# Kernel optimization log

Measured on AMD Instinct MI355X. Metric: run time of the kernel, lower is better.

## Reference

```python
import jax, jax.numpy as jnp
import numpy as np

FFT_LEN = 512
HOP_LEN = 256
N_BLOCK = 4
N_BIN = FFT_LEN // 2 + 1  # 257
STATE_FACTOR = 0.99999
ALPHA_E = 0.7
BETA_F = 0.1
BATCH = 4096
N_MIC = 1


def setup_inputs() -> dict:
    key = jax.random.key(0)
    ks = jax.random.split(key, 7)
    return {
        "mic": jax.random.normal(ks[0], (BATCH, HOP_LEN, N_MIC), jnp.float32),
        "loudspeaker_buffer": jax.random.normal(ks[1], (BATCH, (N_BLOCK + 1) * HOP_LEN), jnp.float32),
        "phi_e": jax.random.uniform(ks[2], (BATCH, N_BIN, N_MIC), jnp.float32),
        "phi_f": jax.random.uniform(ks[3], (BATCH, N_BIN, N_BLOCK, N_MIC), jnp.float32),
        "P1": jax.random.uniform(ks[4], (BATCH, N_BIN, N_BLOCK, N_MIC), jnp.float32),
        "H_post_real": 0.1 * jax.random.normal(ks[5], (BATCH, N_BIN, N_BLOCK, N_MIC), jnp.float32),
        "H_post_imag": 0.1 * jax.random.normal(ks[6], (BATCH, N_BIN, N_BLOCK, N_MIC), jnp.float32),
    }


def reference(mic, loudspeaker_buffer, phi_e, phi_f, P1, H_post_real, H_post_imag):
    B = mic.shape[0]
    sf2 = STATE_FACTOR * STATE_FACTOR
    H_post = jax.lax.complex(H_post_real, H_post_imag)  # [B, n_bin, n_block, n_mic]

    # STFT of loudspeaker buffer: rectangular window, center=False -> n_block frames
    frame_idx = jnp.arange(N_BLOCK)[:, None] * HOP_LEN + jnp.arange(FFT_LEN)[None, :]
    frames = loudspeaker_buffer[:, frame_idx]              # [B, n_block, fft_len]
    X = jnp.swapaxes(jnp.fft.rfft(frames, axis=-1), 1, 2)  # [B, n_bin, n_block]

    # zero-padded rFFT of mic frame
    zpad = jnp.zeros((B, FFT_LEN - HOP_LEN, N_MIC), mic.dtype)
    fd_mic = jnp.fft.rfft(jnp.concatenate([zpad, mic], axis=1), n=FFT_LEN, axis=1)  # [B, n_bin, n_mic]

    H_prior = H_post
    # a-priori feedback estimate
    fd_fb_hat = jnp.sum(X[..., None] * H_prior, axis=2)                     # [B, n_bin, n_mic]
    est_fb = jnp.fft.irfft(fd_fb_hat, FFT_LEN, axis=1)[:, HOP_LEN:, :]      # [B, hop, n_mic]
    fd_est_fb = jnp.fft.rfft(jnp.concatenate([zpad, est_fb], axis=1), n=FFT_LEN, axis=1)
    E = fd_mic - fd_est_fb                                                  # [B, n_bin, n_mic]

    phi_e = ALPHA_E * phi_e + (1.0 - ALPHA_E) * jnp.abs(E) ** 2

    # Kalman gain
    phi_f = BETA_F * phi_f + (1.0 - BETA_F) * jnp.abs(H_prior) ** 2
    phi_n = (1.0 - sf2) * phi_f
    Xr = jnp.abs(X) ** 2                                                    # [B, n_bin, n_block]
    U = Xr[..., None] * P1                                                  # [B, n_bin, n_block, n_mic]
    R = U + 2.0 * phi_e[:, :, None, :] + 1e-10
    K = P1 * jnp.conj(X)[..., None] / R                                     # [B, n_bin, n_block, n_mic]
    P0 = jax.lax.stop_gradient(P1) - 0.5 * jax.lax.stop_gradient(jnp.abs(K) ** 2 * R)
    P1_new = sf2 * P0 + phi_n  # state update (not part of returned output)

    # filter update via gradient-constrained overlap-save
    dH = jnp.fft.irfft(K * E[:, :, None, :], FFT_LEN, axis=1)               # [B, fft_len, n_block, n_mic]
    mask = (jnp.arange(FFT_LEN) < HOP_LEN).astype(dH.dtype)[None, :, None, None]
    fd_dH = jnp.fft.rfft(dH * mask, n=FFT_LEN, axis=1)                      # [B, n_bin, n_block, n_mic]
    H_post_new = STATE_FACTOR * (H_prior + fd_dH)

    # a-posteriori feedback estimate and enhanced frame
    fd_fb_hat2 = jnp.sum(X[..., None] * H_post_new, axis=2)
    est_fb2 = jnp.fft.irfft(fd_fb_hat2, FFT_LEN, axis=1)[:, HOP_LEN:, :]
    enhanced = mic - est_fb2                                                # [B, hop, n_mic]
    return enhanced
```

## Files before the change

kernel.cpp:

```cpp
#include <hip/hip_runtime.h>
#include <math.h>

#define SF 0.99999f
#define PI2 6.283185307179586476925f
#define SWZ(c) ((c) ^ (((c) >> 4) & 15))
#define LDSFENCE() asm volatile("" ::: "memory")

template<int SGN>
__device__ __forceinline__ void twmul(float& ur, float& ui, float c, float s) {
    const float ss = (SGN < 0) ? -s : s;
    const float r = ur * c - ui * ss;
    const float i = ui * c + ur * ss;
    ur = r; ui = i;
}

template<int SGN>
__device__ __forceinline__ void bfly8(float* ur, float* ui) {
    const float C2 = 0.70710678118654752440f;
    float ar[4], ai[4], br[4], bi[4];
#pragma unroll
    for (int m = 0; m < 4; ++m) {
        ar[m] = ur[m] + ur[m + 4]; ai[m] = ui[m] + ui[m + 4];
        br[m] = ur[m] - ur[m + 4]; bi[m] = ui[m] - ui[m + 4];
    }
    float b1r, b1i, b2r, b2i, b3r, b3i;
    if (SGN < 0) {
        b1r = C2 * (br[1] + bi[1]); b1i = C2 * (bi[1] - br[1]);
        b2r = bi[2];                b2i = -br[2];
        b3r = C2 * (bi[3] - br[3]); b3i = -C2 * (br[3] + bi[3]);
    } else {
        b1r = C2 * (br[1] - bi[1]); b1i = C2 * (bi[1] + br[1]);
        b2r = -bi[2];               b2i = br[2];
        b3r = -C2 * (br[3] + bi[3]); b3i = C2 * (br[3] - bi[3]);
    }
    const float e0r = ar[0] + ar[2], e0i = ai[0] + ai[2];
    const float e1r = ar[0] - ar[2], e1i = ai[0] - ai[2];
    const float o0r = ar[1] + ar[3], o0i = ai[1] + ai[3];
    const float o1r = ar[1] - ar[3], o1i = ai[1] - ai[3];
    ur[0] = e0r + o0r; ui[0] = e0i + o0i;
    ur[4] = e0r - o0r; ui[4] = e0i - o0i;
    if (SGN < 0) { ur[2] = e1r + o1i; ui[2] = e1i - o1r; ur[6] = e1r - o1i; ui[6] = e1i + o1r; }
    else         { ur[2] = e1r - o1i; ui[2] = e1i + o1r; ur[6] = e1r + o1i; ui[6] = e1i - o1r; }
    const float f0r = br[0] + b2r, f0i = bi[0] + b2i;
    const float f1r = br[0] - b2r, f1i = bi[0] - b2i;
    const float g0r = b1r + b3r, g0i = b1i + b3i;
    const float g1r = b1r - b3r, g1i = b1i - b3i;
    ur[1] = f0r + g0r; ui[1] = f0i + g0i;
    ur[5] = f0r - g0r; ui[5] = f0i - g0i;
    if (SGN < 0) { ur[3] = f1r + g1i; ui[3] = f1i - g1r; ur[7] = f1r - g1i; ui[7] = f1i + g1r; }
    else         { ur[3] = f1r - g1i; ui[3] = f1i + g1r; ur[7] = f1r + g1i; ui[7] = f1i - g1r; }
}

template<int SGN>
__device__ __forceinline__ void fft512w(float* ur, float* ui,
                                        float2* __restrict__ buf,
                                        const float2* __restrict__ tw2,
                                        const float2* __restrict__ tw3,
                                        int t) {
    bfly8<SGN>(ur, ui);
    LDSFENCE();
#pragma unroll
    for (int m = 0; m < 8; ++m) buf[SWZ(8 * t + m)] = make_float2(ur[m], ui[m]);
    LDSFENCE();
#pragma unroll
    for (int m = 0; m < 8; ++m) { const float2 v = buf[SWZ(t + 64 * m)]; ur[m] = v.x; ui[m] = v.y; }
    const int k2 = t & 7;
#pragma unroll
    for (int m = 1; m < 8; ++m) { const float2 w = tw2[m * 8 + k2]; twmul<SGN>(ur[m], ui[m], w.x, w.y); }
    bfly8<SGN>(ur, ui);
    const int jj = ((t >> 3) << 6) + k2;
    LDSFENCE();
#pragma unroll
    for (int m = 0; m < 8; ++m) buf[SWZ(jj + 8 * m)] = make_float2(ur[m], ui[m]);
    LDSFENCE();
#pragma unroll
    for (int m = 0; m < 8; ++m) { const float2 v = buf[SWZ(t + 64 * m)]; ur[m] = v.x; ui[m] = v.y; }
#pragma unroll
    for (int m = 1; m < 8; ++m) { const float2 w = tw3[m * 64 + t]; twmul<SGN>(ur[m], ui[m], w.x, w.y); }
    bfly8<SGN>(ur, ui);
    LDSFENCE();
}

__global__ __launch_bounds__(256, 2) void pbfd_kernel(
    const float* __restrict__ g_mic,
    const float* __restrict__ g_lsb,
    const float* __restrict__ g_phie,
    const float* __restrict__ g_p1,
    const float* __restrict__ g_hr,
    const float* __restrict__ g_hi,
    float* __restrict__ g_out,
    int B) {
    __shared__ float2 tw2[64];
    __shared__ float2 tw3[512];
    __shared__ float2 xch[4][512];
    __shared__ float nyq[4][14];

    const int tid = threadIdx.x;
    const int w = tid >> 6;
    const int t = tid & 63;
    const int elem = blockIdx.x * 4 + w;
    const int ec = (elem < B) ? elem : (B - 1);
    const int ml = (64 - t) & 63;

    float u[20];
    {
        const float* lb = g_lsb + (size_t)ec * 1280;
#pragma unroll
        for (int m = 0; m < 20; ++m) u[m] = lb[t + 64 * m];
    }
    float hr_[4][4], hi_[4][4];
    {
        const float4* hr4 = (const float4*)g_hr + (size_t)ec * 257;
        const float4* hi4 = (const float4*)g_hi + (size_t)ec * 257;
#pragma unroll
        for (int m = 0; m < 4; ++m) {
            const float4 a = hr4[t + 64 * m];
            hr_[0][m] = a.x; hr_[1][m] = a.y; hr_[2][m] = a.z; hr_[3][m] = a.w;
        }
#pragma unroll
        for (int m = 0; m < 4; ++m) {
            const float4 b = hi4[t + 64 * m];
            hi_[0][m] = b.x; hi_[1][m] = b.y; hi_[2][m] = b.z; hi_[3][m] = b.w;
        }
    }
    float mv[4];
    {
        const float* mp = g_mic + (size_t)ec * 256;
#pragma unroll
        for (int q = 0; q < 4; ++q) mv[q] = mp[t + 64 * q];
    }
    float phv[4];
    {
        const float* php = g_phie + (size_t)ec * 257;
#pragma unroll
        for (int m = 0; m < 4; ++m) phv[m] = php[t + 64 * m];
    }
    float4 p1q[4];
    {
        const float4* p14 = (const float4*)g_p1 + (size_t)ec * 257;
#pragma unroll
        for (int m = 0; m < 4; ++m) p1q[m] = p14[t + 64 * m];
    }
    float4 hnl = make_float4(0.f, 0.f, 0.f, 0.f), pnl = make_float4(0.f, 0.f, 0.f, 0.f);
    float ph256 = 0.f;
    if (t == 0) {
        hnl = ((const float4*)g_hr)[(size_t)ec * 257 + 256];
        pnl = ((const float4*)g_p1)[(size_t)ec * 257 + 256];
        ph256 = g_phie[(size_t)ec * 257 + 256];
    }

    for (int e = tid; e < 512; e += 256) {
        const int m = e >> 6, tt = e & 63;
        float s, c;
        sincosf(PI2 * (float)(m * tt) * (1.0f / 512.0f), &s, &c);
        tw3[e] = make_float2(c, s);
    }
    if (tid < 64) {
        const int m = tid >> 3, k = tid & 7;
        float s, c;
        sincosf(PI2 * (float)(m * k) * (1.0f / 64.0f), &s, &c);
        tw2[tid] = make_float2(c, s);
    }
    __syncthreads();

    float2* buf = &xch[w][0];
    float* ny = &nyq[w][0];
    if (t == 0) {
        ny[4] = hnl.x; ny[5] = hnl.y; ny[6] = hnl.z; ny[7] = hnl.w;
        ny[8] = pnl.x; ny[9] = pnl.y; ny[10] = pnl.z; ny[11] = pnl.w;
        ny[12] = ph256;
    }
    LDSFENCE();

    float xr[4][4], xi[4][4];
#pragma unroll
    for (int pr = 0; pr < 2; ++pr) {
        float ur[8], ui[8];
#pragma unroll
        for (int m = 0; m < 8; ++m) { ur[m] = u[8 * pr + m]; ui[m] = u[8 * pr + m + 4]; }
        fft512w<-1>(ur, ui, buf, tw2, tw3, t);
#pragma unroll
        for (int m = 0; m < 4; ++m) {
            float zmr = __shfl(ur[7 - m], ml);
            float zmi = __shfl(ui[7 - m], ml);
            if (t == 0) {
                zmr = (m == 0) ? ur[0] : ur[8 - m];
                zmi = (m == 0) ? ui[0] : ui[8 - m];
            }
            xr[2 * pr][m]     = 0.5f * (ur[m] + zmr);
            xi[2 * pr][m]     = 0.5f * (ui[m] - zmi);
            xr[2 * pr + 1][m] = 0.5f * (ui[m] + zmi);
            xi[2 * pr + 1][m] = -0.5f * (ur[m] - zmr);
        }
        if (t == 0) { ny[0 + 2 * pr] = ur[4]; ny[1 + 2 * pr] = ui[4]; }
        LDSFENCE();
    }

    auto sum_ifft = [&](float o4[4]) {
        float ur[8], ui[8];
#pragma unroll
        for (int m = 0; m < 4; ++m) {
            float cr = 0.f, ci = 0.f;
#pragma unroll
            for (int j = 0; j < 4; ++j) {
                cr += xr[j][m] * hr_[j][m] - xi[j][m] * hi_[j][m];
                ci += xr[j][m] * hi_[j][m] + xi[j][m] * hr_[j][m];
            }
            ur[m] = cr; ui[m] = ci;
        }
#pragma unroll
        for (int m = 4; m < 8; ++m) {
            const float cr = __shfl(ur[7 - m], ml);
            const float ci = __shfl(ui[7 - m], ml);
            ur[m] = cr; ui[m] = -ci;
        }
        if (t == 0) {
            ur[5] = ur[3]; ui[5] = -ui[3];
            ur[6] = ur[2]; ui[6] = -ui[2];
            ur[7] = ur[1]; ui[7] = -ui[1];
            float cn = 0.f;
#pragma unroll
            for (int j = 0; j < 4; ++j) cn += ny[j] * ny[4 + j];
            ur[4] = cn; ui[4] = 0.f;
        }
        fft512w<1>(ur, ui, buf, tw2, tw3, t);
#pragma unroll
        for (int q = 0; q < 4; ++q) o4[q] = ur[4 + q] * (1.0f / 512.0f);
    };

    float d4[4];
    {
        float o4[4];
        sum_ifft(o4);
#pragma unroll
        for (int q = 0; q < 4; ++q) d4[q] = mv[q] - o4[q];
    }

    float er[4], ei[4];
    {
        float ur[8], ui[8];
#pragma unroll
        for (int m = 0; m < 4; ++m) { ur[m] = 0.f; ui[m] = 0.f; }
#pragma unroll
        for (int q = 0; q < 4; ++q) { ur[4 + q] = d4[q]; ui[4 + q] = 0.f; }
        fft512w<-1>(ur, ui, buf, tw2, tw3, t);
#pragma unroll
        for (int m = 0; m < 4; ++m) { er[m] = ur[m]; ei[m] = ui[m]; }
        if (t == 0) {
            const float en = ur[4];
            ny[13] = en;
            ny[12] = 0.7f * ny[12] + 0.3f * en * en;
        }
        LDSFENCE();
    }

    float pe[4];
#pragma unroll
    for (int m = 0; m < 4; ++m)
        pe[m] = 0.7f * phv[m] + 0.3f * (er[m] * er[m] + ei[m] * ei[m]);

#pragma unroll
    for (int pr = 0; pr < 2; ++pr) {
        const int j0 = 2 * pr, j1 = 2 * pr + 1;
        float ur[8], ui[8], gr[4], gi[4];
#pragma unroll
        for (int m = 0; m < 4; ++m) {
            const float pa = pr ? p1q[m].z : p1q[m].x;
            const float pb = pr ? p1q[m].w : p1q[m].y;
            const float xxa = xr[j0][m] * xr[j0][m] + xi[j0][m] * xi[j0][m];
            const float Ra = xxa * pa + 2.f * pe[m] + 1e-10f;
            const float ia = 1.f / Ra;
            const float kra = pa * xr[j0][m] * ia, kia = -pa * xi[j0][m] * ia;
            const float a_r = kra * er[m] - kia * ei[m];
            const float a_i = kra * ei[m] + kia * er[m];
            const float xxb = xr[j1][m] * xr[j1][m] + xi[j1][m] * xi[j1][m];
            const float Rb = xxb * pb + 2.f * pe[m] + 1e-10f;
            const float ib = 1.f / Rb;
            const float krb = pb * xr[j1][m] * ib, kib = -pb * xi[j1][m] * ib;
            const float b_r = krb * er[m] - kib * ei[m];
            const float b_i = krb * ei[m] + kib * er[m];
            ur[m] = a_r - b_i;  ui[m] = a_i + b_r;
            gr[m] = a_r + b_i;  gi[m] = b_r - a_i;
        }
#pragma unroll
        for (int m = 4; m < 8; ++m) {
            ur[m] = __shfl(gr[7 - m], ml);
            ui[m] = __shfl(gi[7 - m], ml);
        }
        if (t == 0) {
            ur[5] = gr[3]; ui[5] = gi[3];
            ur[6] = gr[2]; ui[6] = gi[2];
            ur[7] = gr[1]; ui[7] = gi[1];
            const float xn0 = ny[j0], xn1 = ny[j1];
            const float pn0 = ny[8 + j0], pn1 = ny[8 + j1];
            const float en = ny[13], pen = ny[12];
            const float Rn0 = xn0 * xn0 * pn0 + 2.f * pen + 1e-10f;
            const float Rn1 = xn1 * xn1 * pn1 + 2.f * pen + 1e-10f;
            ur[4] = pn0 * xn0 / Rn0 * en;
            ui[4] = pn1 * xn1 / Rn1 * en;
        }
        fft512w<1>(ur, ui, buf, tw2, tw3, t);
#pragma unroll
        for (int m = 0; m < 4; ++m) { ur[m] *= (1.0f / 512.0f); ui[m] *= (1.0f / 512.0f); }
#pragma unroll
        for (int m = 4; m < 8; ++m) { ur[m] = 0.f; ui[m] = 0.f; }
        fft512w<-1>(ur, ui, buf, tw2, tw3, t);
#pragma unroll
        for (int m = 0; m < 4; ++m) {
            float zmr = __shfl(ur[7 - m], ml);
            float zmi = __shfl(ui[7 - m], ml);
            if (t == 0) {
                zmr = (m == 0) ? ur[0] : ur[8 - m];
                zmi = (m == 0) ? ui[0] : ui[8 - m];
            }
            const float f0r = 0.5f * (ur[m] + zmr), f0i = 0.5f * (ui[m] - zmi);
            const float f1r = 0.5f * (ui[m] + zmi), f1i = -0.5f * (ur[m] - zmr);
            hr_[j0][m] = SF * (hr_[j0][m] + f0r);
            hi_[j0][m] = SF * (hi_[j0][m] + f0i);
            hr_[j1][m] = SF * (hr_[j1][m] + f1r);
            hi_[j1][m] = SF * (hi_[j1][m] + f1i);
        }
        if (t == 0) {
            ny[4 + j0] = SF * (ny[4 + j0] + ur[4]);
            ny[4 + j1] = SF * (ny[4 + j1] + ui[4]);
        }
        LDSFENCE();
    }

    {
        float o4[4];
        sum_ifft(o4);
        if (elem < B) {
            float* op = g_out + (size_t)elem * 256;
#pragma unroll
            for (int q = 0; q < 4; ++q) op[t + 64 * q] = mv[q] - o4[q];
        }
    }
}

extern "C" void kernel_launch(void* const* d_in, const int* in_sizes, int n_in,
                              void* d_out, int out_size, void* d_ws, size_t ws_size,
                              hipStream_t stream) {
    const float* mic  = (const float*)d_in[0];
    const float* lsb  = (const float*)d_in[1];
    const float* phie = (const float*)d_in[2];
    const float* p1   = (const float*)d_in[4];
    const float* hr   = (const float*)d_in[5];
    const float* hi   = (const float*)d_in[6];
    float* out = (float*)d_out;

    const int B = in_sizes[0] / 256;
    const int blocks = (B + 3) / 4;
    pbfd_kernel<<<blocks, 256, 0, stream>>>(mic, lsb, phie, p1, hr, hi, out, B);
}
```

Baseline: 40.37 us.

## Interleave paired FFTs with dual LDS buffers and stagger wave start times

Adds a dual FFT routine that runs two independent 512-point FFTs at once using separate LDS scratch buffers. The loudspeaker STFT and the two filter-update FFT pairs now use it instead of running back to back, giving more instruction-level parallelism and overlapped LDS latency. It also raises the launch-bounds occupancy hint from 2 to 3 blocks per SM and inserts per-wave s_sleep offsets so waves do not all hit the same phase at once. The costs are doubled LDS scratch per wave, more live registers under a tighter register cap (risk of spills), and added sleep latency.

```diff
diff --git a/kernel.cpp b/kernel.cpp
--- a/kernel.cpp
+++ b/kernel.cpp
@@ -81,7 +81,58 @@
     LDSFENCE();
 }
 
-__global__ __launch_bounds__(256, 2) void pbfd_kernel(
+template<int SGN>
+__device__ __forceinline__ void fft512w_dual(float* urA, float* uiA,
+                                             float* urB, float* uiB,
+                                             float2* __restrict__ bufA,
+                                             float2* __restrict__ bufB,
+                                             const float2* __restrict__ tw2,
+                                             const float2* __restrict__ tw3,
+                                             int t) {
+    bfly8<SGN>(urA, uiA);
+    bfly8<SGN>(urB, uiB);
+    LDSFENCE();
+#pragma unroll
+    for (int m = 0; m < 8; ++m) bufA[SWZ(8 * t + m)] = make_float2(urA[m], uiA[m]);
+#pragma unroll
+    for (int m = 0; m < 8; ++m) bufB[SWZ(8 * t + m)] = make_float2(urB[m], uiB[m]);
+    LDSFENCE();
+#pragma unroll
+    for (int m = 0; m < 8; ++m) { const float2 v = bufA[SWZ(t + 64 * m)]; urA[m] = v.x; uiA[m] = v.y; }
+#pragma unroll
+    for (int m = 0; m < 8; ++m) { const float2 v = bufB[SWZ(t + 64 * m)]; urB[m] = v.x; uiB[m] = v.y; }
+    const int k2 = t & 7;
+#pragma unroll
+    for (int m = 1; m < 8; ++m) {
+        const float2 wv = tw2[m * 8 + k2];
+        twmul<SGN>(urA[m], uiA[m], wv.x, wv.y);
+        twmul<SGN>(urB[m], uiB[m], wv.x, wv.y);
+    }
+    bfly8<SGN>(urA, uiA);
+    bfly8<SGN>(urB, uiB);
+    const int jj = ((t >> 3) << 6) + k2;
+    LDSFENCE();
+#pragma unroll
+    for (int m = 0; m < 8; ++m) bufA[SWZ(jj + 8 * m)] = make_float2(urA[m], uiA[m]);
+#pragma unroll
+    for (int m = 0; m < 8; ++m) bufB[SWZ(jj + 8 * m)] = make_float2(urB[m], uiB[m]);
+    LDSFENCE();
+#pragma unroll
+    for (int m = 0; m < 8; ++m) { const float2 v = bufA[SWZ(t + 64 * m)]; urA[m] = v.x; uiA[m] = v.y; }
+#pragma unroll
+    for (int m = 0; m < 8; ++m) { const float2 v = bufB[SWZ(t + 64 * m)]; urB[m] = v.x; uiB[m] = v.y; }
+#pragma unroll
+    for (int m = 1; m < 8; ++m) {
+        const float2 wv = tw3[m * 64 + t];
+        twmul<SGN>(urA[m], uiA[m], wv.x, wv.y);
+        twmul<SGN>(urB[m], uiB[m], wv.x, wv.y);
+    }
+    bfly8<SGN>(urA, uiA);
+    bfly8<SGN>(urB, uiB);
+    LDSFENCE();
+}
+
+__global__ __launch_bounds__(256, 3) void pbfd_kernel(
     const float* __restrict__ g_mic,
     const float* __restrict__ g_lsb,
     const float* __restrict__ g_phie,
@@ -92,7 +143,7 @@
     int B) {
     __shared__ float2 tw2[64];
     __shared__ float2 tw3[512];
-    __shared__ float2 xch[4][512];
+    __shared__ float2 xch[4][2][512];
     __shared__ float nyq[4][14];
 
     const int tid = threadIdx.x;
@@ -108,6 +159,12 @@
 #pragma unroll
         for (int m = 0; m < 20; ++m) u[m] = lb[t + 64 * m];
     }
+    float mv[4];
+    {
+        const float* mp = g_mic + (size_t)ec * 256;
+#pragma unroll
+        for (int q = 0; q < 4; ++q) mv[q] = mp[t + 64 * q];
+    }
     float hr_[4][4], hi_[4][4];
     {
         const float4* hr4 = (const float4*)g_hr + (size_t)ec * 257;
@@ -122,12 +179,6 @@
             const float4 b = hi4[t + 64 * m];
             hi_[0][m] = b.x; hi_[1][m] = b.y; hi_[2][m] = b.z; hi_[3][m] = b.w;
         }
-    }
-    float mv[4];
-    {
-        const float* mp = g_mic + (size_t)ec * 256;
-#pragma unroll
-        for (int q = 0; q < 4; ++q) mv[q] = mp[t + 64 * q];
     }
     float phv[4];
     {
@@ -163,7 +214,8 @@
     }
     __syncthreads();
 
-    float2* buf = &xch[w][0];
+    float2* bufA = &xch[w][0][0];
+    float2* bufB = &xch[w][1][0];
     float* ny = &nyq[w][0];
     if (t == 0) {
         ny[4] = hnl.x; ny[5] = hnl.y; ny[6] = hnl.z; ny[7] = hnl.w;
@@ -172,27 +224,47 @@
     }
     LDSFENCE();
 
+    switch ((w + ((blockIdx.x & 1) << 2)) & 7) {
+        case 1: __builtin_amdgcn_s_sleep(2); break;
+        case 2: __builtin_amdgcn_s_sleep(4); break;
+        case 3: __builtin_amdgcn_s_sleep(6); break;
+        case 4: __builtin_amdgcn_s_sleep(8); break;
+        case 5: __builtin_amdgcn_s_sleep(10); break;
+        case 6: __builtin_amdgcn_s_sleep(12); break;
+        case 7: __builtin_amdgcn_s_sleep(14); break;
+        default: break;
+    }
+
     float xr[4][4], xi[4][4];
-#pragma unroll
-    for (int pr = 0; pr < 2; ++pr) {
-        float ur[8], ui[8];
-#pragma unroll
-        for (int m = 0; m < 8; ++m) { ur[m] = u[8 * pr + m]; ui[m] = u[8 * pr + m + 4]; }
-        fft512w<-1>(ur, ui, buf, tw2, tw3, t);
-#pragma unroll
-        for (int m = 0; m < 4; ++m) {
-            float zmr = __shfl(ur[7 - m], ml);
-            float zmi = __shfl(ui[7 - m], ml);
-            if (t == 0) {
-                zmr = (m == 0) ? ur[0] : ur[8 - m];
-                zmi = (m == 0) ? ui[0] : ui[8 - m];
-            }
-            xr[2 * pr][m]     = 0.5f * (ur[m] + zmr);
-            xi[2 * pr][m]     = 0.5f * (ui[m] - zmi);
-            xr[2 * pr + 1][m] = 0.5f * (ui[m] + zmi);
-            xi[2 * pr + 1][m] = -0.5f * (ur[m] - zmr);
-        }
-        if (t == 0) { ny[0 + 2 * pr] = ur[4]; ny[1 + 2 * pr] = ui[4]; }
+    {
+        float urA[8], uiA[8], urB[8], uiB[8];
+#pragma unroll
+        for (int m = 0; m < 8; ++m) {
+            urA[m] = u[m];     uiA[m] = u[m + 4];
+            urB[m] = u[m + 8]; uiB[m] = u[m + 12];
+        }
+        fft512w_dual<-1>(urA, uiA, urB, uiB, bufA, bufB, tw2, tw3, t);
+#pragma unroll
+        for (int m = 0; m < 4; ++m) {
+            float zmr = __shfl(urA[7 - m], ml);
+            float zmi = __shfl(uiA[7 - m], ml);
+            if (t == 0) { zmr = (m == 0) ? urA[0] : urA[8 - m]; zmi = (m == 0) ? uiA[0] : uiA[8 - m]; }
+            xr[0][m] = 0.5f * (urA[m] + zmr);
+            xi[0][m] = 0.5f * (uiA[m] - zmi);
+            xr[1][m] = 0.5f * (uiA[m] + zmi);
+            xi[1][m] = -0.5f * (urA[m] - zmr);
+        }
+#pragma unroll
+        for (int m = 0; m < 4; ++m) {
+            float zmr = __shfl(urB[7 - m], ml);
+            float zmi = __shfl(uiB[7 - m], ml);
+            if (t == 0) { zmr = (m == 0) ? urB[0] : urB[8 - m]; zmi = (m == 0) ? uiB[0] : uiB[8 - m]; }
+            xr[2][m] = 0.5f * (urB[m] + zmr);
+            xi[2][m] = 0.5f * (uiB[m] - zmi);
+            xr[3][m] = 0.5f * (uiB[m] + zmi);
+            xi[3][m] = -0.5f * (urB[m] - zmr);
+        }
+        if (t == 0) { ny[0] = urA[4]; ny[1] = uiA[4]; ny[2] = urB[4]; ny[3] = uiB[4]; }
         LDSFENCE();
     }
 
@@ -223,7 +295,7 @@
             for (int j = 0; j < 4; ++j) cn += ny[j] * ny[4 + j];
             ur[4] = cn; ui[4] = 0.f;
         }
-        fft512w<1>(ur, ui, buf, tw2, tw3, t);
+        fft512w<1>(ur, ui, bufA, tw2, tw3, t);
 #pragma unroll
         for (int q = 0; q < 4; ++q) o4[q] = ur[4 + q] * (1.0f / 512.0f);
     };
@@ -243,7 +315,7 @@
         for (int m = 0; m < 4; ++m) { ur[m] = 0.f; ui[m] = 0.f; }
 #pragma unroll
         for (int q = 0; q < 4; ++q) { ur[4 + q] = d4[q]; ui[4 + q] = 0.f; }
-        fft512w<-1>(ur, ui, buf, tw2, tw3, t);
+        fft512w<-1>(ur, ui, bufA, tw2, tw3, t);
 #pragma unroll
         for (int m = 0; m < 4; ++m) { er[m] = ur[m]; ei[m] = ui[m]; }
         if (t == 0) {
@@ -259,70 +331,104 @@
     for (int m = 0; m < 4; ++m)
         pe[m] = 0.7f * phv[m] + 0.3f * (er[m] * er[m] + ei[m] * ei[m]);
 
-#pragma unroll
-    for (int pr = 0; pr < 2; ++pr) {
-        const int j0 = 2 * pr, j1 = 2 * pr + 1;
-        float ur[8], ui[8], gr[4], gi[4];
-#pragma unroll
-        for (int m = 0; m < 4; ++m) {
-            const float pa = pr ? p1q[m].z : p1q[m].x;
-            const float pb = pr ? p1q[m].w : p1q[m].y;
-            const float xxa = xr[j0][m] * xr[j0][m] + xi[j0][m] * xi[j0][m];
-            const float Ra = xxa * pa + 2.f * pe[m] + 1e-10f;
-            const float ia = 1.f / Ra;
-            const float kra = pa * xr[j0][m] * ia, kia = -pa * xi[j0][m] * ia;
-            const float a_r = kra * er[m] - kia * ei[m];
-            const float a_i = kra * ei[m] + kia * er[m];
-            const float xxb = xr[j1][m] * xr[j1][m] + xi[j1][m] * xi[j1][m];
-            const float Rb = xxb * pb + 2.f * pe[m] + 1e-10f;
-            const float ib = 1.f / Rb;
-            const float krb = pb * xr[j1][m] * ib, kib = -pb * xi[j1][m] * ib;
-            const float b_r = krb * er[m] - kib * ei[m];
-            const float b_i = krb * ei[m] + kib * er[m];
-            ur[m] = a_r - b_i;  ui[m] = a_i + b_r;
-            gr[m] = a_r + b_i;  gi[m] = b_r - a_i;
+    {
+        float urA[8], uiA[8], urB[8], uiB[8];
+        float grA[4], giA[4], grB[4], giB[4];
+#pragma unroll
+        for (int m = 0; m < 4; ++m) {
+            const float xx0 = xr[0][m] * xr[0][m] + xi[0][m] * xi[0][m];
+            const float R0 = xx0 * p1q[m].x + 2.f * pe[m] + 1e-10f;
+            const float i0 = 1.f / R0;
+            const float kr0 = p1q[m].x * xr[0][m] * i0, ki0 = -p1q[m].x * xi[0][m] * i0;
+            const float a_r = kr0 * er[m] - ki0 * ei[m];
+            const float a_i = kr0 * ei[m] + ki0 * er[m];
+            const float xx1 = xr[1][m] * xr[1][m] + xi[1][m] * xi[1][m];
+            const float R1 = xx1 * p1q[m].y + 2.f * pe[m] + 1e-10f;
+            const float i1 = 1.f / R1;
+            const float kr1 = p1q[m].y * xr[1][m] * i1, ki1 = -p1q[m].y * xi[1][m] * i1;
+            const float b_r = kr1 * er[m] - ki1 * ei[m];
+            const float b_i = kr1 * ei[m] + ki1 * er[m];
+            urA[m] = a_r - b_i;  uiA[m] = a_i + b_r;
+            grA[m] = a_r + b_i;  giA[m] = b_r - a_i;
+
+            const float xx2 = xr[2][m] * xr[2][m] + xi[2][m] * xi[2][m];
+            const float R2 = xx2 * p1q[m].z + 2.f * pe[m] + 1e-10f;
+            const float i2 = 1.f / R2;
+            const float kr2 = p1q[m].z * xr[2][m] * i2, ki2 = -p1q[m].z * xi[2][m] * i2;
+            const float c_r = kr2 * er[m] - ki2 * ei[m];
+            const float c_i = kr2 * ei[m] + ki2 * er[m];
+            const float xx3 = xr[3][m] * xr[3][m] + xi[3][m] * xi[3][m];
+            const float R3 = xx3 * p1q[m].w + 2.f * pe[m] + 1e-10f;
+            const float i3 = 1.f / R3;
+            const float kr3 = p1q[m].w * xr[3][m] * i3, ki3 = -p1q[m].w * xi[3][m] * i3;
+            const float d_r = kr3 * er[m] - ki3 * ei[m];
+            const float d_i = kr3 * ei[m] + ki3 * er[m];
+            urB[m] = c_r - d_i;  uiB[m] = c_i + d_r;
+            grB[m] = c_r + d_i;  giB[m] = d_r - c_i;
         }
 #pragma unroll
         for (int m = 4; m < 8; ++m) {
-            ur[m] = __shfl(gr[7 - m], ml);
-            ui[m] = __shfl(gi[7 - m], ml);
+            urA[m] = __shfl(grA[7 - m], ml);
+            uiA[m] = __shfl(giA[7 - m], ml);
+            urB[m] = __shfl(grB[7 - m], ml);
+            uiB[m] = __shfl(giB[7 - m], ml);
         }
         if (t == 0) {
-            ur[5] = gr[3]; ui[5] = gi[3];
-            ur[6] = gr[2]; ui[6] = gi[2];
-            ur[7] = gr[1]; ui[7] = gi[1];
-            const float xn0 = ny[j0], xn1 = ny[j1];
-            const float pn0 = ny[8 + j0], pn1 = ny[8 + j1];
+            urA[5] = grA[3]; uiA[5] = giA[3];
+            urA[6] = grA[2]; uiA[6] = giA[2];
+            urA[7] = grA[1]; uiA[7] = giA[1];
+            urB[5] = grB[3]; uiB[5] = giB[3];
+            urB[6] = grB[2]; uiB[6] = giB[2];
+            urB[7] = grB[1]; uiB[7] = giB[1];
             const float en = ny[13], pen = ny[12];
-            const float Rn0 = xn0 * xn0 * pn0 + 2.f * pen + 1e-10f;
-            const float Rn1 = xn1 * xn1 * pn1 + 2.f * pen + 1e-10f;
-            ur[4] = pn0 * xn0 / Rn0 * en;
-            ui[4] = pn1 * xn1 / Rn1 * en;
-        }
-        fft512w<1>(ur, ui, buf, tw2, tw3, t);
-#pragma unroll
-        for (int m = 0; m < 4; ++m) { ur[m] *= (1.0f / 512.0f); ui[m] *= (1.0f / 512.0f); }
-#pragma unroll
-        for (int m = 4; m < 8; ++m) { ur[m] = 0.f; ui[m] = 0.f; }
-        fft512w<-1>(ur, ui, buf, tw2, tw3, t);
-#pragma unroll
-        for (int m = 0; m < 4; ++m) {
-            float zmr = __shfl(ur[7 - m], ml);
-            float zmi = __shfl(ui[7 - m], ml);
-            if (t == 0) {
-                zmr = (m == 0) ? ur[0] : ur[8 - m];
-                zmi = (m == 0) ? ui[0] : ui[8 - m];
+#pragma unroll
+            for (int j = 0; j < 4; ++j) {
+                const float xnj = ny[j], pnj = ny[8 + j];
+                const float Rn = xnj * xnj * pnj + 2.f * pen + 1e-10f;
+                const float ke = pnj * xnj / Rn * en;
+                if (j == 0) urA[4] = ke;
+                else if (j == 1) uiA[4] = ke;
+                else if (j == 2) urB[4] = ke;
+                else uiB[4] = ke;
             }
-            const float f0r = 0.5f * (ur[m] + zmr), f0i = 0.5f * (ui[m] - zmi);
-            const float f1r = 0.5f * (ui[m] + zmi), f1i = -0.5f * (ur[m] - zmr);
-            hr_[j0][m] = SF * (hr_[j0][m] + f0r);
-            hi_[j0][m] = SF * (hi_[j0][m] + f0i);
-            hr_[j1][m] = SF * (hr_[j1][m] + f1r);
-            hi_[j1][m] = SF * (hi_[j1][m] + f1i);
+        }
+        fft512w_dual<1>(urA, uiA, urB, uiB, bufA, bufB, tw2, tw3, t);
+#pragma unroll
+        for (int m = 0; m < 4; ++m) {
+            urA[m] *= (1.0f / 512.0f); uiA[m] *= (1.0f / 512.0f);
+            urB[m] *= (1.0f / 512.0f); uiB[m] *= (1.0f / 512.0f);
+        }
+#pragma unroll
+        for (int m = 4; m < 8; ++m) {
+            urA[m] = 0.f; uiA[m] = 0.f;
+            urB[m] = 0.f; uiB[m] = 0.f;
+        }
+        fft512w_dual<-1>(urA, uiA, urB, uiB, bufA, bufB, tw2, tw3, t);
+#pragma unroll
+        for (int m = 0; m < 4; ++m) {
+            float zmr = __shfl(urA[7 - m], ml);
+            float zmi = __shfl(uiA[7 - m], ml);
+            if (t == 0) { zmr = (m == 0) ? urA[0] : urA[8 - m]; zmi = (m == 0) ? uiA[0] : uiA[8 - m]; }
+            hr_[0][m] = SF * (hr_[0][m] + 0.5f * (urA[m] + zmr));
+            hi_[0][m] = SF * (hi_[0][m] + 0.5f * (uiA[m] - zmi));
+            hr_[1][m] = SF * (hr_[1][m] + 0.5f * (uiA[m] + zmi));
+            hi_[1][m] = SF * (hi_[1][m] - 0.5f * (urA[m] - zmr));
+        }
+#pragma unroll
+        for (int m = 0; m < 4; ++m) {
+            float zmr = __shfl(urB[7 - m], ml);
+            float zmi = __shfl(uiB[7 - m], ml);
+            if (t == 0) { zmr = (m == 0) ? urB[0] : urB[8 - m]; zmi = (m == 0) ? uiB[0] : uiB[8 - m]; }
+            hr_[2][m] = SF * (hr_[2][m] + 0.5f * (urB[m] + zmr));
+            hi_[2][m] = SF * (hi_[2][m] + 0.5f * (uiB[m] - zmi));
+            hr_[3][m] = SF * (hr_[3][m] + 0.5f * (uiB[m] + zmi));
+            hi_[3][m] = SF * (hi_[3][m] - 0.5f * (urB[m] - zmr));
         }
         if (t == 0) {
-            ny[4 + j0] = SF * (ny[4 + j0] + ur[4]);
-            ny[4 + j1] = SF * (ny[4 + j1] + ui[4]);
+            ny[4] = SF * (ny[4] + urA[4]);
+            ny[5] = SF * (ny[5] + uiA[4]);
+            ny[6] = SF * (ny[6] + urB[4]);
+            ny[7] = SF * (ny[7] + uiB[4]);
         }
         LDSFENCE();
     }
```

Measured after the change: 59.59 us. 1.48x slower.
